# Kernel tuning notes

Measured on AMD Instinct MI355X. Metric: run time of the kernel, lower is better.

## Reference

```python
import jax, jax.numpy as jnp
import numpy as np

MAX_VALUE = 127.0  # signed 8-bit: 2**(8-1)-1


def _quantize_int8(t, amax):
    # per-tensor symmetric quantization: round(x * 127/amax), clamped to [-127, 127]
    scale = MAX_VALUE / amax
    return jnp.clip(jnp.round(t * scale), -MAX_VALUE, MAX_VALUE).astype(jnp.int8)


def setup_inputs() -> dict:
    key = jax.random.key(0)
    k1, k2, k3 = jax.random.split(key, 3)
    N, K, M = 8192, 4096, 4096
    x = jax.random.normal(k1, (N, K), dtype=jnp.float32)
    weight = jax.random.normal(k2, (M, K), dtype=jnp.float32) * (1.0 / np.sqrt(K))
    bias = jax.random.normal(k3, (M,), dtype=jnp.float32) * (1.0 / np.sqrt(K))
    return {"x": x, "weight": weight, "bias": bias}


def reference(x, weight, bias):
    # amax from max-abs calibration (per-tensor), as TensorQuantizer would hold
    amax = jnp.max(jnp.abs(x))
    amax_w = jnp.max(jnp.abs(weight))
    qi = _quantize_int8(x, amax)          # [N, K] int8
    qw = _quantize_int8(weight, amax_w)   # [M, K] int8
    acc = jnp.matmul(qi.astype(jnp.int32), qw.astype(jnp.int32).T)  # [N, M] int32
    # dequant: output / ((max/amax) * (max/amax_w)), then bias
    dequant = (amax * amax_w) / (MAX_VALUE * MAX_VALUE)
    return acc.astype(jnp.float32) * dequant + bias
```

## Files before the change

### kernel.cpp

```cpp
#include <hip/hip_runtime.h>

#define K_DIM 4096
#define N_DIM 8192
#define M_DIM 4096

typedef int v4i __attribute__((ext_vector_type(4)));

__global__ void amax2_kernel(const float4* __restrict__ x,
                             const float4* __restrict__ w,
                             unsigned* __restrict__ scal) {
  const int XB = 2048, WB = 1024;
  const float4* p;
  int n4, b, nb;
  unsigned* out;
  if (blockIdx.x < XB) {
    p = x; n4 = N_DIM * K_DIM / 4; out = scal + 0; b = blockIdx.x; nb = XB;
  } else {
    p = w; n4 = M_DIM * K_DIM / 4; out = scal + 1; b = blockIdx.x - XB; nb = WB;
  }
  int tid = b * blockDim.x + threadIdx.x;
  int stride = nb * blockDim.x;
  float m = 0.f;
  for (int i = tid; i < n4; i += stride) {
    float4 v = p[i];
    m = fmaxf(m, fmaxf(fmaxf(fabsf(v.x), fabsf(v.y)),
                       fmaxf(fabsf(v.z), fabsf(v.w))));
  }
#pragma unroll
  for (int off = 32; off > 0; off >>= 1)
    m = fmaxf(m, __shfl_down(m, off));
  __shared__ float sm[4];
  int lane = threadIdx.x & 63, wv = threadIdx.x >> 6;
  if (lane == 0) sm[wv] = m;
  __syncthreads();
  if (threadIdx.x == 0) {
    m = fmaxf(fmaxf(sm[0], sm[1]), fmaxf(sm[2], sm[3]));
    atomicMax(out, __float_as_uint(m));
  }
}

__device__ __forceinline__ unsigned pack4(float4 v, float s) {
  int q0 = (int)fminf(fmaxf(rintf(v.x * s), -127.f), 127.f);
  int q1 = (int)fminf(fmaxf(rintf(v.y * s), -127.f), 127.f);
  int q2 = (int)fminf(fmaxf(rintf(v.z * s), -127.f), 127.f);
  int q3 = (int)fminf(fmaxf(rintf(v.w * s), -127.f), 127.f);
  return (unsigned)(q0 & 255) | ((unsigned)(q1 & 255) << 8) |
         ((unsigned)(q2 & 255) << 16) | ((unsigned)(q3 & 255) << 24);
}

__global__ void quant2_kernel(const float4* __restrict__ x,
                              const float4* __restrict__ w,
                              unsigned* __restrict__ qx, unsigned* __restrict__ qw,
                              const unsigned* __restrict__ scal) {
  const int XB = 2048, WB = 1024;
  const float4* in;
  unsigned* out;
  int n4, b, nb;
  float amax;
  if (blockIdx.x < XB) {
    in = x; out = qx; n4 = N_DIM * K_DIM / 4; b = blockIdx.x; nb = XB;
    amax = __uint_as_float(scal[0]);
  } else {
    in = w; out = qw; n4 = M_DIM * K_DIM / 4; b = blockIdx.x - XB; nb = WB;
    amax = __uint_as_float(scal[1]);
  }
  float s = 127.0f / amax;
  int tid = b * blockDim.x + threadIdx.x;
  int stride = nb * blockDim.x;
  for (int i = tid; i < n4; i += stride) out[i] = pack4(in[i], s);
}

__device__ __forceinline__ void gld_lds16(const void* g, void* l) {
  __builtin_amdgcn_global_load_lds(
      (const __attribute__((address_space(1))) void*)g,
      (__attribute__((address_space(3))) void*)l, 16, 0, 0);
}

__global__ __launch_bounds__(512, 2) void gemm_i8(
    const signed char* __restrict__ A,
    const signed char* __restrict__ B,
    const float* __restrict__ bias,
    float* __restrict__ out,
    const unsigned* __restrict__ scal)
{
  __shared__ signed char lds[2][2][256 * 128];

  const int tid = threadIdx.x;
  const int lane = tid & 63;
  const int w = tid >> 6;
  const int wm = w >> 2;
  const int wn = w & 3;
  const long r0 = (long)blockIdx.x * 256;
  const long c0 = (long)blockIdx.y * 256;

  const int srow = tid >> 3;
  const int gcol = ((tid & 7) ^ (srow & 7)) * 16;
  const signed char* ga = A + (r0 + srow) * K_DIM + gcol;
  const signed char* gb = B + (c0 + srow) * K_DIM + gcol;
  const int ldst = tid * 16;

  v4i acc[8][4];
#pragma unroll
  for (int i = 0; i < 8; ++i)
#pragma unroll
    for (int j = 0; j < 4; ++j) acc[i][j] = (v4i){0, 0, 0, 0};

  const int fr = lane & 15;
  const int fq = lane >> 4;
  const int sa = fr & 7;

  auto STAGE = [&](int t, int buf) {
    const long ko = (long)t * 128;
    signed char* la = &lds[buf][0][0];
    signed char* lb = &lds[buf][1][0];
#pragma unroll
    for (int p = 0; p < 4; ++p)
      gld_lds16(ga + (long)p * 64 * K_DIM + ko, la + p * 8192 + ldst);
#pragma unroll
    for (int p = 0; p < 4; ++p)
      gld_lds16(gb + (long)p * 64 * K_DIM + ko, lb + p * 8192 + ldst);
  };

  auto COMPUTE = [&](int buf) {
    const signed char* la = &lds[buf][0][0];
    const signed char* lb = &lds[buf][1][0];
#pragma unroll
    for (int ks = 0; ks < 2; ++ks) {
      const int co = ((ks * 4 + fq) ^ sa) * 16;
      v4i bv[4];
#pragma unroll
      for (int nf = 0; nf < 4; ++nf)
        bv[nf] = *(const v4i*)(lb + (wn * 64 + nf * 16 + fr) * 128 + co);
#pragma unroll
      for (int mh = 0; mh < 2; ++mh) {
        v4i av[4];
#pragma unroll
        for (int mi = 0; mi < 4; ++mi)
          av[mi] =
              *(const v4i*)(la + (wm * 128 + mh * 64 + mi * 16 + fr) * 128 + co);
        __builtin_amdgcn_s_setprio(1);
#pragma unroll
        for (int mi = 0; mi < 4; ++mi)
#pragma unroll
          for (int nf = 0; nf < 4; ++nf)
            acc[mh * 4 + mi][nf] = __builtin_amdgcn_mfma_i32_16x16x64_i8(
                av[mi], bv[nf], acc[mh * 4 + mi][nf], 0, 0, 0);
        __builtin_amdgcn_s_setprio(0);
      }
    }
  };

  const int NT = K_DIM / 128;
  STAGE(0, 0);
  STAGE(1, 1);
  for (int t = 0; t < NT - 1; ++t) {
    asm volatile("s_waitcnt vmcnt(8)" ::: "memory");
    __builtin_amdgcn_s_barrier();
    COMPUTE(t & 1);
    __builtin_amdgcn_s_barrier();
    if (t + 2 < NT) STAGE(t + 2, t & 1);
  }
  asm volatile("s_waitcnt vmcnt(0)" ::: "memory");
  __builtin_amdgcn_s_barrier();
  COMPUTE((NT - 1) & 1);

  const float dq =
      (__uint_as_float(scal[0]) * __uint_as_float(scal[1])) / 16129.0f;
  float bs[4];
#pragma unroll
  for (int nf = 0; nf < 4; ++nf) bs[nf] = bias[c0 + wn * 64 + nf * 16 + fr];

#pragma unroll
  for (int mf = 0; mf < 8; ++mf) {
    const long rbase = r0 + wm * 128 + mf * 16 + fq * 4;
#pragma unroll
    for (int nf = 0; nf < 4; ++nf) {
      const long c = c0 + wn * 64 + nf * 16 + fr;
#pragma unroll
      for (int t = 0; t < 4; ++t) {
        out[(rbase + t) * (long)M_DIM + c] = (float)acc[mf][nf][t] * dq + bs[nf];
      }
    }
  }
}

extern "C" void kernel_launch(void* const* d_in, const int* in_sizes, int n_in,
                              void* d_out, int out_size, void* d_ws, size_t ws_size,
                              hipStream_t stream) {
  const float* x = (const float*)d_in[0];
  const float* wt = (const float*)d_in[1];
  const float* bias = (const float*)d_in[2];
  float* out = (float*)d_out;

  unsigned* scal = (unsigned*)d_ws;
  signed char* qx = (signed char*)d_ws + 256;
  signed char* qw = qx + (long)N_DIM * K_DIM;

  hipMemsetAsync(d_ws, 0, 16, stream);

  amax2_kernel<<<3072, 256, 0, stream>>>((const float4*)x, (const float4*)wt,
                                         scal);
  quant2_kernel<<<3072, 256, 0, stream>>>((const float4*)x, (const float4*)wt,
                                          (unsigned*)qx, (unsigned*)qw, scal);

  dim3 grid(N_DIM / 256, M_DIM / 256);
  gemm_i8<<<grid, 512, 0, stream>>>(qx, qw, bias, out, scal);
}
```

Measured before the change: 434.0 us.

## Restructure int8 GEMM into 4-stage 64-wide K pipeline with XCD-aware tile mapping

Replaces the double-buffered 128-wide K loop with a four-buffer ring of 64-wide K tiles, prefetching three tiles ahead. Global-to-LDS loads are interleaved between two MFMA half-phases, with finer barriers and vmcnt guards. The launch changes to a 1D grid whose block index is remapped so that each XCD works on a contiguous 8x8 patch of output tiles, which should improve L2 reuse. This adds more barriers per K step and more complex waitcnt bookkeeping, which could raise synchronisation overhead or create ordering hazards.

```diff
diff --git a/kernel.cpp b/kernel.cpp
--- a/kernel.cpp
+++ b/kernel.cpp
@@ -83,20 +83,26 @@
     float* __restrict__ out,
     const unsigned* __restrict__ scal)
 {
-  __shared__ signed char lds[2][2][256 * 128];
+  __shared__ signed char lds[4][2][128 * 128];
 
   const int tid = threadIdx.x;
   const int lane = tid & 63;
   const int w = tid >> 6;
   const int wm = w >> 2;
   const int wn = w & 3;
-  const long r0 = (long)blockIdx.x * 256;
-  const long c0 = (long)blockIdx.y * 256;
-
-  const int srow = tid >> 3;
-  const int gcol = ((tid & 7) ^ (srow & 7)) * 16;
-  const signed char* ga = A + (r0 + srow) * K_DIM + gcol;
-  const signed char* gb = B + (c0 + srow) * K_DIM + gcol;
+
+  const int bid = blockIdx.x;
+  const int xcd = bid & 7, idx = bid >> 3;
+  const int bx = (xcd & 3) * 8 + (idx & 7);
+  const int by = (xcd >> 2) * 8 + (idx >> 3);
+  const long r0 = (long)bx * 256;
+  const long c0 = (long)by * 256;
+
+  const int u = (tid & 7) ^ ((tid >> 3) & 7);
+  const long sR = (long)(u >> 2) * 128 + (tid >> 3);
+  const int scol = (u & 3) * 16;
+  const signed char* gA = A + (r0 + sR) * K_DIM + scol;
+  const signed char* gB = B + (c0 + sR) * K_DIM + scol;
   const int ldst = tid * 16;
 
   v4i acc[8][4];
@@ -107,62 +113,71 @@
 
   const int fr = lane & 15;
   const int fq = lane >> 4;
-  const int sa = fr & 7;
-
-  auto STAGE = [&](int t, int buf) {
-    const long ko = (long)t * 128;
-    signed char* la = &lds[buf][0][0];
-    signed char* lb = &lds[buf][1][0];
-#pragma unroll
-    for (int p = 0; p < 4; ++p)
-      gld_lds16(ga + (long)p * 64 * K_DIM + ko, la + p * 8192 + ldst);
-#pragma unroll
-    for (int p = 0; p < 4; ++p)
-      gld_lds16(gb + (long)p * 64 * K_DIM + ko, lb + p * 8192 + ldst);
+  const int sw = fr & 7;
+
+  const int aoff = fr * 128 + (((wm << 2) | fq) ^ sw) * 16;
+  const int boff = ((wn & 1) * 64 + fr) * 128 + ((((wn >> 1) << 2) | fq) ^ sw) * 16;
+
+  auto STAGE = [&](int T, int p) {
+    signed char* la = &lds[T & 3][0][0];
+    signed char* lb = &lds[T & 3][1][0];
+    gld_lds16(gA + (long)p * 64 * K_DIM + T * 64, la + p * 8192 + ldst);
+    gld_lds16(gB + (long)p * 64 * K_DIM + T * 64, lb + p * 8192 + ldst);
   };
 
-  auto COMPUTE = [&](int buf) {
-    const signed char* la = &lds[buf][0][0];
-    const signed char* lb = &lds[buf][1][0];
-#pragma unroll
-    for (int ks = 0; ks < 2; ++ks) {
-      const int co = ((ks * 4 + fq) ^ sa) * 16;
-      v4i bv[4];
+  auto TILE = [&](int T, bool stg, int guard) {
+    const signed char* la = &lds[T & 3][0][0];
+    const signed char* lb = &lds[T & 3][1][0];
+    v4i bv[4], a0[4], a1[4];
+#pragma unroll
+    for (int nf = 0; nf < 4; ++nf)
+      bv[nf] = *(const v4i*)(lb + boff + nf * 2048);
+#pragma unroll
+    for (int mi = 0; mi < 4; ++mi)
+      a0[mi] = *(const v4i*)(la + aoff + mi * 2048);
+    if (stg) STAGE(T + 3, 0);
+    __builtin_amdgcn_s_barrier();
+    asm volatile("s_waitcnt lgkmcnt(0)" ::: "memory");
+    __builtin_amdgcn_s_setprio(1);
+#pragma unroll
+    for (int mi = 0; mi < 4; ++mi)
 #pragma unroll
       for (int nf = 0; nf < 4; ++nf)
-        bv[nf] = *(const v4i*)(lb + (wn * 64 + nf * 16 + fr) * 128 + co);
-#pragma unroll
-      for (int mh = 0; mh < 2; ++mh) {
-        v4i av[4];
-#pragma unroll
-        for (int mi = 0; mi < 4; ++mi)
-          av[mi] =
-              *(const v4i*)(la + (wm * 128 + mh * 64 + mi * 16 + fr) * 128 + co);
-        __builtin_amdgcn_s_setprio(1);
-#pragma unroll
-        for (int mi = 0; mi < 4; ++mi)
-#pragma unroll
-          for (int nf = 0; nf < 4; ++nf)
-            acc[mh * 4 + mi][nf] = __builtin_amdgcn_mfma_i32_16x16x64_i8(
-                av[mi], bv[nf], acc[mh * 4 + mi][nf], 0, 0, 0);
-        __builtin_amdgcn_s_setprio(0);
-      }
-    }
+        acc[mi][nf] = __builtin_amdgcn_mfma_i32_16x16x64_i8(a0[mi], bv[nf],
+                                                            acc[mi][nf], 0, 0, 0);
+    __builtin_amdgcn_s_setprio(0);
+    __builtin_amdgcn_s_barrier();
+#pragma unroll
+    for (int mi = 0; mi < 4; ++mi)
+      a1[mi] = *(const v4i*)(la + aoff + 8192 + mi * 2048);
+    if (stg) STAGE(T + 3, 1);
+    if (guard == 8) asm volatile("s_waitcnt vmcnt(8)" ::: "memory");
+    else if (guard == 4) asm volatile("s_waitcnt vmcnt(4)" ::: "memory");
+    else if (guard == 0) asm volatile("s_waitcnt vmcnt(0)" ::: "memory");
+    __builtin_amdgcn_s_barrier();
+    asm volatile("s_waitcnt lgkmcnt(0)" ::: "memory");
+    __builtin_amdgcn_s_setprio(1);
+#pragma unroll
+    for (int mi = 0; mi < 4; ++mi)
+#pragma unroll
+      for (int nf = 0; nf < 4; ++nf)
+        acc[4 + mi][nf] = __builtin_amdgcn_mfma_i32_16x16x64_i8(
+            a1[mi], bv[nf], acc[4 + mi][nf], 0, 0, 0);
+    __builtin_amdgcn_s_setprio(0);
+    __builtin_amdgcn_s_barrier();
   };
 
-  const int NT = K_DIM / 128;
-  STAGE(0, 0);
-  STAGE(1, 1);
-  for (int t = 0; t < NT - 1; ++t) {
-    asm volatile("s_waitcnt vmcnt(8)" ::: "memory");
-    __builtin_amdgcn_s_barrier();
-    COMPUTE(t & 1);
-    __builtin_amdgcn_s_barrier();
-    if (t + 2 < NT) STAGE(t + 2, t & 1);
-  }
-  asm volatile("s_waitcnt vmcnt(0)" ::: "memory");
+  const int NT = K_DIM / 64;
+#pragma unroll
+  for (int T = 0; T < 3; ++T) { STAGE(T, 0); STAGE(T, 1); }
+  asm volatile("s_waitcnt vmcnt(8)" ::: "memory");
   __builtin_amdgcn_s_barrier();
-  COMPUTE((NT - 1) & 1);
+
+#pragma unroll 1
+  for (int T = 0; T + 4 <= NT; ++T) TILE(T, true, 8);
+  TILE(NT - 3, false, 4);
+  TILE(NT - 2, false, 0);
+  TILE(NT - 1, false, -1);
 
   const float dq =
       (__uint_as_float(scal[0]) * __uint_as_float(scal[1])) / 16129.0f;
@@ -203,6 +218,5 @@
   quant2_kernel<<<3072, 256, 0, stream>>>((const float4*)x, (const float4*)wt,
                                           (unsigned*)qx, (unsigned*)qw, scal);
 
-  dim3 grid(N_DIM / 256, M_DIM / 256);
-  gemm_i8<<<grid, 512, 0, stream>>>(qx, qw, bias, out, scal);
-}
+  gemm_i8<<<512, 512, 0, stream>>>(qx, qw, bias, out, scal);
+}
```

Result: no change. 434.6 us (+0.1%).
